# Kernel optimization log

Hardware: AMD Instinct MI355X
Metric: run time of the kernel (lower is better)

## Reference

```python
import jax, jax.numpy as jnp
import numpy as np

B, C, H, W = 8, 64, 64, 64
CI = 32  # inter_channels = in_channels // 2
EPS = 1e-5


def conv1x1(x, w, b=None):
    # x: (b,c,h,w), w: (o,c) -> (b,o,h,w)
    y = jnp.einsum('bchw,oc->bohw', x, w)
    if b is not None:
        y = y + b[None, :, None, None]
    return y


def maxpool2x2(x):
    b, c, h, w = x.shape
    return x.reshape(b, c, h // 2, 2, w // 2, 2).max(axis=(3, 5))


def setup_inputs() -> dict:
    key = jax.random.key(0)
    ks = jax.random.split(key, 12)
    s = 0.05
    return {
        'x': jax.random.normal(ks[0], (B, C, H, W), jnp.float32),
        'theta_w': jax.random.normal(ks[1], (CI, C), jnp.float32) * s,
        'theta_b': jax.random.normal(ks[2], (CI,), jnp.float32) * s,
        'phi_w': jax.random.normal(ks[3], (CI, C), jnp.float32) * s,
        'phi_b': jax.random.normal(ks[4], (CI,), jnp.float32) * s,
        'psi_w': jax.random.normal(ks[5], (CI, C), jnp.float32) * s,
        'psi_b': jax.random.normal(ks[6], (CI,), jnp.float32) * s,
        'cp_w': jax.random.normal(ks[7], (2 * CI,), jnp.float32) * s,  # concat_project 1x1, no bias
        'W_w': jax.random.normal(ks[8], (C, CI + 1), jnp.float32) * s,
        'W_b': jax.random.normal(ks[9], (C,), jnp.float32) * s,
        'bn_gamma': jax.random.normal(ks[10], (C,), jnp.float32) * s + 1.0,
        'bn_beta': jax.random.normal(ks[11], (C,), jnp.float32) * s,
    }


def reference(x, theta_w, theta_b, phi_w, phi_b, psi_w, psi_b, cp_w, W_w, W_b, bn_gamma, bn_beta):
    b = x.shape[0]
    # psi / phi branches get 2x2 maxpool (sub_sample=True default)
    psi_x = maxpool2x2(conv1x1(x, psi_w, psi_b)).reshape(b, CI, -1)      # (b,ci,M)
    psi_x = psi_x.transpose(0, 2, 1)                                     # (b,M,ci)
    theta_x = conv1x1(x, theta_w, theta_b).reshape(b, CI, -1)            # (b,ci,N)
    phi_x = maxpool2x2(conv1x1(x, phi_w, phi_b)).reshape(b, CI, -1)      # (b,ci,M)
    # concat_project(cat[theta_i, phi_j]) + ReLU == relu(w1.theta_i + w2.phi_j)
    w1, w2 = cp_w[:CI], cp_w[CI:]
    a = jnp.einsum('bcn,c->bn', theta_x, w1)                             # (b,N)
    bb = jnp.einsum('bcm,c->bm', phi_x, w2)                              # (b,M)
    f = jax.nn.relu(a[:, :, None] + bb[:, None, :])                      # (b,N,M)
    M = f.shape[-1]
    f_div_C = f / float(M)
    y = jnp.matmul(f_div_C, psi_x)                                       # (b,N,ci)
    y = y.transpose(0, 2, 1).reshape(b, CI, H, W)
    # r_structure_type='zero' -> zero structure channel
    structure_feat = jnp.zeros((b, 1, H, W), y.dtype)
    y = jnp.concatenate([y, structure_feat], axis=1)                     # (b,ci+1,H,W)
    wy = conv1x1(y, W_w, W_b)                                            # (b,C,H,W)
    # BatchNorm2d, training-mode batch stats, biased variance
    mu = wy.mean(axis=(0, 2, 3), keepdims=True)
    var = wy.var(axis=(0, 2, 3), keepdims=True)
    wy = (wy - mu) * jax.lax.rsqrt(var + EPS)
    wy = wy * bn_gamma[None, :, None, None] + bn_beta[None, :, None, None]
    return wy + x
```

## Files before the change

### kernel.cpp

```cpp
#include <hip/hip_runtime.h>

#define OFF_A    0
#define OFF_BB   32768
#define OFF_RK   40960
#define OFF_U    57344
#define OFF_T1   581632
#define OFF_T2   1106432
#define OFF_KK   1631232
#define OFF_MP1  1664000
#define OFF_MP2  1664512
#define OFF_HC   1665024
#define OFF_HS   1673224
#define OFF_HS2  1681424
#define OFF_BAR  1689624

__device__ __forceinline__ void stg(float* p, float v) {
    __hip_atomic_store(p, v, __ATOMIC_RELAXED, __HIP_MEMORY_SCOPE_AGENT);
}
__device__ __forceinline__ float ldg1(const float* p) {
    return __hip_atomic_load(p, __ATOMIC_RELAXED, __HIP_MEMORY_SCOPE_AGENT);
}
__device__ __forceinline__ void stgi(int* p, int v) {
    __hip_atomic_store(p, v, __ATOMIC_RELAXED, __HIP_MEMORY_SCOPE_AGENT);
}
__device__ __forceinline__ int ldgi(const int* p) {
    return __hip_atomic_load(p, __ATOMIC_RELAXED, __HIP_MEMORY_SCOPE_AGENT);
}
__device__ __forceinline__ void stgu(unsigned* p, unsigned v) {
    __hip_atomic_store(p, v, __ATOMIC_RELAXED, __HIP_MEMORY_SCOPE_AGENT);
}
__device__ __forceinline__ unsigned ldgu(const unsigned* p) {
    return __hip_atomic_load(p, __ATOMIC_RELAXED, __HIP_MEMORY_SCOPE_AGENT);
}

__global__ __launch_bounds__(1024) void kA(
    const float* __restrict__ x, const float* __restrict__ theta_w,
    const float* __restrict__ theta_b, const float* __restrict__ phi_w,
    const float* __restrict__ phi_b, const float* __restrict__ psi_w,
    const float* __restrict__ psi_b, const float* __restrict__ cp_w,
    const float* __restrict__ Ww, float* __restrict__ ws)
{
    __shared__ float sh[7524];
    const int tid = threadIdx.x;
    const int bid = blockIdx.x;
    const int b   = bid >> 5;
    const int sub = bid & 31;
    unsigned* bars = (unsigned*)(ws + OFF_BAR);
    float* sA2 = sh + 7396;

    {
        if (bid == 0 && tid == 0) {
            for (int i = 0; i < 8; ++i) stgu(&bars[(i + 1) << 5], 0u);
        }
        if (tid < 97) {
            int e = sub*97 + tid;
            if (e < 1025)      stg(&ws[OFF_HC  + b*1025 + e], 0.0f);
            else if (e < 2050) stg(&ws[OFF_HS  + b*1025 + e - 1025], 0.0f);
            else if (e < 3075) stg(&ws[OFF_HS2 + b*1025 + e - 2050], 0.0f);
        }
        float* sm   = sh;
        float* sth  = sh + 4160;
        float* spsi = sh + 4228;
        float* sWw  = sh + 5284;
        for (int e = tid; e < 2048; e += 1024) {
            int i = e >> 6, c = e & 63;
            sm[i*130 + 2*c]     = phi_w[e];
            sm[i*130 + 2*c + 1] = psi_w[e];
        }
        for (int e = tid; e < 2048; e += 1024)
            sWw[(e >> 5)*33 + (e & 31)] = Ww[(e >> 5)*33 + (e & 31)];
        if (tid < 64) {
            float s = 0;
            for (int i = 0; i < 32; ++i) s += cp_w[i]*theta_w[i*64 + tid];
            sth[tid] = s;
        } else if (tid == 64) {
            float s = 0;
            for (int i = 0; i < 32; ++i) s += cp_w[i]*theta_b[i];
            sth[64] = s;
        }
        __syncthreads();
        if (bid == 0 && tid == 0) {
            stgu(&bars[288], 0x5A5A5A5Au);
            stgu(&bars[289], 0xA5A5A5A5u);
        }
        int i = tid & 31;
        int mIdx = tid >> 5;
        int m = (sub << 5) + mIdx;
        int ph = m >> 5, pw = m & 31;
        const float* xb = x + b*262144 + ph*128 + pw*2;
        const float2* wrow = (const float2*)(sm + i*130);
        float tb = sth[64];
        float p0=0,p1=0,p2=0,p3=0,s0=0,s1=0,s2=0,s3=0;
        float a0=tb,a1=tb,a2=tb,a3=tb;
        #pragma unroll 8
        for (int c = 0; c < 64; ++c) {
            float2 xa = *(const float2*)(xb + c*4096);
            float2 xc = *(const float2*)(xb + c*4096 + 64);
            float2 w  = wrow[c];
            float st  = sth[c];
            p0 += xa.x*w.x; p1 += xa.y*w.x; p2 += xc.x*w.x; p3 += xc.y*w.x;
            s0 += xa.x*w.y; s1 += xa.y*w.y; s2 += xc.x*w.y; s3 += xc.y*w.y;
            a0 += xa.x*st;  a1 += xa.y*st;  a2 += xc.x*st;  a3 += xc.y*st;
        }
        float pv = fmaxf(fmaxf(p0,p1), fmaxf(p2,p3)) + phi_b[i];
        float sv = fmaxf(fmaxf(s0,s1), fmaxf(s2,s3)) + psi_b[i];
        spsi[mIdx*33 + i] = sv;
        float v = pv * cp_w[32 + i];
        v += __shfl_xor(v, 16, 32);
        v += __shfl_xor(v,  8, 32);
        v += __shfl_xor(v,  4, 32);
        v += __shfl_xor(v,  2, 32);
        v += __shfl_xor(v,  1, 32);
        if (i == 0) {
            stg(&ws[OFF_BB + (b<<10) + m], v);
            int nb = (b<<12) + ph*128 + pw*2;
            ws[OFF_A + nb]      = a0;
            ws[OFF_A + nb + 1]  = a1;
            ws[OFF_A + nb + 64] = a2;
            ws[OFF_A + nb + 65] = a3;
            int nl = pw*2;
            sA2[nl]      = a0;
            sA2[nl + 1]  = a1;
            sA2[nl + 64] = a2;
            sA2[nl + 65] = a3;
        }
        __syncthreads();
        #pragma unroll
        for (int rep = 0; rep < 2; ++rep) {
            int o  = (tid >> 5) + (rep << 5);
            int ml = tid & 31;
            const float* pr = &spsi[ml*33];
            const float* wr = &sWw[o*33];
            float u = 0;
            #pragma unroll
            for (int i2 = 0; i2 < 32; ++i2) u += pr[i2]*wr[i2];
            stg(&ws[OFF_U + (((b<<6) + o)<<10) + (sub<<5) + ml], u);
        }
    }
    __syncthreads();
    if (tid == 0) {
        while ((ldgu(&bars[288]) ^ ldgu(&bars[289])) != 0xFFFFFFFFu)
            __builtin_amdgcn_s_sleep(2);
        unsigned* ctr = bars + ((b + 1) << 5);
        __hip_atomic_fetch_add(ctr, 1u, __ATOMIC_RELAXED,
                               __HIP_MEMORY_SCOPE_AGENT);
        while (ldgu(ctr) < 32u) __builtin_amdgcn_s_sleep(2);
    }
    __syncthreads();

    {
        float* sb = sh;
        sb[tid] = ldg1(&ws[OFF_BB + (b<<10) + tid]);
        __syncthreads();
        {
            int ml = tid >> 5, jl = tid & 31;
            int m = (sub << 5) + ml;
            float vv = sb[m];
            int cnt = 0;
            for (int s = 0; s < 32; ++s) {
                int j = jl + (s << 5);
                float u = sb[j];
                cnt += (u > vv || (u == vv && j < m)) ? 1 : 0;
            }
            cnt += __shfl_xor(cnt,  1, 32);
            cnt += __shfl_xor(cnt,  2, 32);
            cnt += __shfl_xor(cnt,  4, 32);
            cnt += __shfl_xor(cnt,  8, 32);
            cnt += __shfl_xor(cnt, 16, 32);
            if (jl == 0)
                stgi(&((int*)ws)[OFF_RK + (b<<10) + m], cnt);
        }
        {
            int l = tid >> 3, jl = tid & 7;
            int n = (sub << 7) + l;
            float av = sA2[l];
            float tt = -av;
            const float2* sb2 = (const float2*)sb;
            int cnt = 0;
            for (int s = 0; s < 64; ++s) {
                float2 u = sb2[jl + (s << 3)];
                cnt += (u.x > tt) ? 1 : 0;
                cnt += (u.y > tt) ? 1 : 0;
            }
            cnt += __shfl_xor(cnt, 1, 8);
            cnt += __shfl_xor(cnt, 2, 8);
            cnt += __shfl_xor(cnt, 4, 8);
            if (jl == 0) {
                ((int*)ws)[OFF_KK + (b<<12) + n] = cnt;
                atomicAdd(&ws[OFF_HC + b*1025 + cnt], 1.0f);
                atomicAdd(&ws[OFF_HS + b*1025 + cnt], av);
                atomicAdd(&ws[OFF_HS2 + b*1025 + cnt], av*av);
            }
        }
    }
    __syncthreads();
    if (tid == 0) {
        unsigned* ctr = bars + ((b + 1) << 5);
        __hip_atomic_fetch_add(ctr, 1u, __ATOMIC_RELAXED,
                               __HIP_MEMORY_SCOPE_AGENT);
        while (ldgu(ctr) < 64u) __builtin_amdgcn_s_sleep(2);
    }
    __syncthreads();

    {
        const int obase = sub << 1;
        float* ssb  = sh;
        float* sU0  = sh + 1024;
        float* sU1  = sh + 2048;
        float* shc  = sh + 3072;
        float* shs  = sh + 4097;
        float* shs2 = sh + 5122;
        float* swp1 = sh + 6148;
        float* swp2 = sh + 6180;
        {
            float bbv = ldg1(&ws[OFF_BB + (b<<10) + tid]);
            int   rk  = ldgi(&((const int*)ws)[OFF_RK + (b<<10) + tid]);
            float u0  = ldg1(&ws[OFF_U + (((b<<6) + obase)<<10) + tid]);
            float u1  = ldg1(&ws[OFF_U + (((b<<6) + obase + 1)<<10) + tid]);
            ssb[rk] = bbv;
            sU0[rk] = u0;
            sU1[rk] = u1;
            shc[tid]  = ldg1(&ws[OFF_HC  + b*1025 + tid]);
            shs[tid]  = ldg1(&ws[OFF_HS  + b*1025 + tid]);
            shs2[tid] = ldg1(&ws[OFF_HS2 + b*1025 + tid]);
            if (tid == 0) {
                shc[1024]  = ldg1(&ws[OFF_HC  + b*1025 + 1024]);
                shs[1024]  = ldg1(&ws[OFF_HS  + b*1025 + 1024]);
                shs2[1024] = ldg1(&ws[OFF_HS2 + b*1025 + 1024]);
            }
        }
        __syncthreads();
        int ch = tid >> 1, o2 = tid & 1;
        int o  = obase + o2;
        int wv = tid >> 6, chl = (tid & 63) >> 1;
        const float* sU = o2 ? sU1 : sU0;
        float p[2], sp[2];
        float s1 = 0, s2 = 0;
        #pragma unroll
        for (int jl = 0; jl < 2; ++jl) {
            int jj = (ch<<1) + jl;
            float v = sU[jj];
            p[jl] = v;
            sp[jl] = ssb[jj]*v;
            s1 += v; s2 += sp[jl];
        }
        float own1 = s1, own2 = s2;
        #pragma unroll
        for (int d = 1; d < 32; d <<= 1) {
            float u1 = __shfl_up(s1, d<<1, 64);
            float u2 = __shfl_up(s2, d<<1, 64);
            if (chl >= d) { s1 += u1; s2 += u2; }
        }
        if (chl == 31) { swp1[(wv<<1)+o2] = s1; swp2[(wv<<1)+o2] = s2; }
        __syncthreads();
        float off1 = 0, off2 = 0;
        for (int w = 0; w < 16; ++w) {
            if (w < wv) { off1 += swp1[(w<<1)+o2]; off2 += swp2[(w<<1)+o2]; }
        }
        float run1 = off1 + s1 - own1;
        float run2 = off2 + s2 - own2;
        float* T1 = ws + OFF_T1 + b*65600;
        float* T2 = ws + OFF_T2 + b*65600;
        if (ch == 0) { T1[o] = 0.0f; T2[o] = 0.0f; }
        const float inv = 1.0f/1024.0f;
        float m1 = 0, m2 = 0;
        #pragma unroll
        for (int jl = 0; jl < 2; ++jl) {
            int k = (ch<<1) + jl + 1;
            run1 += p[jl]; run2 += sp[jl];
            float t1 = run1*inv, t2 = run2*inv;
            T1[(k<<6) + o] = t1;
            T2[(k<<6) + o] = t2;
            float c = shc[k], sa_ = shs[k], sa2 = shs2[k];
            m1 += sa_*t1 + c*t2;
            m2 += (sa2*t1 + 2.0f*sa_*t2)*t1 + c*t2*t2;
        }
        m1 += __shfl_xor(m1,  2, 64); m2 += __shfl_xor(m2,  2, 64);
        m1 += __shfl_xor(m1,  4, 64); m2 += __shfl_xor(m2,  4, 64);
        m1 += __shfl_xor(m1,  8, 64); m2 += __shfl_xor(m2,  8, 64);
        m1 += __shfl_xor(m1, 16, 64); m2 += __shfl_xor(m2, 16, 64);
        m1 += __shfl_xor(m1, 32, 64); m2 += __shfl_xor(m2, 32, 64);
        __syncthreads();
        if (chl == 0) { swp1[(wv<<1)+o2] = m1; swp2[(wv<<1)+o2] = m2; }
        __syncthreads();
        if (tid < 2) {
            float a1 = 0, a2 = 0;
            for (int w = 0; w < 16; ++w) {
                a1 += swp1[(w<<1)+tid]; a2 += swp2[(w<<1)+tid];
            }
            ws[OFF_MP1 + (b<<6) + obase + tid] = a1;
            ws[OFF_MP2 + (b<<6) + obase + tid] = a2;
        }
    }
}

__global__ __launch_bounds__(512) void kB(
    const float* __restrict__ x, const float* __restrict__ Wb,
    const float* __restrict__ gamma, const float* __restrict__ beta,
    const float* __restrict__ ws, float* __restrict__ out)
{
    __shared__ float tile[64*65];
    __shared__ float sa[64];
    __shared__ int   sk[64];
    __shared__ float sA[64];
    __shared__ float sD[64];
    const int tid = threadIdx.x;
    const int b   = blockIdx.x >> 6;
    const int n0  = (blockIdx.x & 63) << 6;
    if (tid < 64) {
        sa[tid] = ws[OFF_A + (b<<12) + n0 + tid];
        sk[tid] = ((const int*)ws)[OFF_KK + (b<<12) + n0 + tid];
        const float Ninv = 1.0f/32768.0f;
        float m1s = 0, m2s = 0;
        #pragma unroll
        for (int b3 = 0; b3 < 8; ++b3) {
            m1s += ws[OFF_MP1 + (b3<<6) + tid];
            m2s += ws[OFF_MP2 + (b3<<6) + tid];
        }
        float m1 = m1s * Ninv;
        float m2 = m2s * Ninv;
        float wb = Wb[tid];
        float mu  = m1 + wb;
        float E2  = m2 + 2.0f*wb*m1 + wb*wb;
        float var = E2 - mu*mu;
        float A = gamma[tid] * rsqrtf(var + 1e-5f);
        sA[tid] = A;
        sD[tid] = beta[tid] + A*(wb - mu);
    }
    __syncthreads();
    const float* T1 = ws + OFF_T1 + b*65600;
    const float* T2 = ws + OFF_T2 + b*65600;
    {
        int o = tid & 63, ng = tid >> 6;
        float Ao = sA[o], Do = sD[o];
        #pragma unroll
        for (int j = 0; j < 8; ++j) {
            int n = (ng << 3) + j;
            int k = sk[n];
            float a = sa[n];
            float t1 = T1[(k<<6) + o];
            float t2 = T2[(k<<6) + o];
            tile[o*65 + n] = Ao*(a*t1 + t2) + Do;
        }
    }
    __syncthreads();
    {
        int n = tid & 63, og = tid >> 6;
        #pragma unroll
        for (int j = 0; j < 8; ++j) {
            int o = (og << 3) + j;
            int idx = ((b<<6) + o)*4096 + n0 + n;
            out[idx] = tile[o*65 + n] + x[idx];
        }
    }
}

extern "C" void kernel_launch(void* const* d_in, const int* in_sizes, int n_in,
                              void* d_out, int out_size, void* d_ws, size_t ws_size,
                              hipStream_t stream)
{
    const float* x       = (const float*)d_in[0];
    const float* theta_w = (const float*)d_in[1];
    const float* theta_b = (const float*)d_in[2];
    const float* phi_w   = (const float*)d_in[3];
    const float* phi_b   = (const float*)d_in[4];
    const float* psi_w   = (const float*)d_in[5];
    const float* psi_b   = (const float*)d_in[6];
    const float* cp_w    = (const float*)d_in[7];
    const float* Ww      = (const float*)d_in[8];
    const float* Wb      = (const float*)d_in[9];
    const float* gamma   = (const float*)d_in[10];
    const float* beta    = (const float*)d_in[11];
    float* ws  = (float*)d_ws;
    float* out = (float*)d_out;

    kA<<<256, 1024, 0, stream>>>(x, theta_w, theta_b, phi_w, phi_b,
                                 psi_w, psi_b, cp_w, Ww, ws);
    kB<<<512, 512, 0, stream>>>(x, Wb, gamma, beta, ws, out);
}
```

Before: 125.6 us.

## Split kA across 512 smaller blocks and interleave T1/T2 as float2

kA now runs 512 blocks of 512 threads. Each block handles 16 pooled positions, and in the prefix-scan phase each block handles one output channel instead of two. Block ids are interleaved across the batch, with matching changes to the per-batch barrier counts and the local A indexing. The T1/T2 tables are merged into one float2 array, so kB's data-dependent gather needs a single 8-byte load per element instead of two scattered loads. The aim is more parallelism and better gather efficiency. The cost is that the spin barriers now wait on twice as many blocks and rely on all 512 blocks being co-resident.

Result: no change. 128.0 us (+1.9%).

```diff
diff --git a/kernel.cpp b/kernel.cpp
--- a/kernel.cpp
+++ b/kernel.cpp
@@ -4,8 +4,7 @@
 #define OFF_BB   32768
 #define OFF_RK   40960
 #define OFF_U    57344
-#define OFF_T1   581632
-#define OFF_T2   1106432
+#define OFF_T12  581632
 #define OFF_KK   1631232
 #define OFF_MP1  1664000
 #define OFF_MP2  1664512
@@ -33,27 +32,27 @@
     return __hip_atomic_load(p, __ATOMIC_RELAXED, __HIP_MEMORY_SCOPE_AGENT);
 }
 
-__global__ __launch_bounds__(1024) void kA(
+__global__ __launch_bounds__(512) void kA(
     const float* __restrict__ x, const float* __restrict__ theta_w,
     const float* __restrict__ theta_b, const float* __restrict__ phi_w,
     const float* __restrict__ phi_b, const float* __restrict__ psi_w,
     const float* __restrict__ psi_b, const float* __restrict__ cp_w,
     const float* __restrict__ Ww, float* __restrict__ ws)
 {
-    __shared__ float sh[7524];
+    __shared__ float sh[6932];
     const int tid = threadIdx.x;
     const int bid = blockIdx.x;
-    const int b   = bid >> 5;
-    const int sub = bid & 31;
+    const int b   = bid & 7;
+    const int sub = bid >> 3;
     unsigned* bars = (unsigned*)(ws + OFF_BAR);
-    float* sA2 = sh + 7396;
+    float* sA2 = sh + 6868;
 
     {
         if (bid == 0 && tid == 0) {
             for (int i = 0; i < 8; ++i) stgu(&bars[(i + 1) << 5], 0u);
         }
-        if (tid < 97) {
-            int e = sub*97 + tid;
+        if (tid < 49) {
+            int e = sub*49 + tid;
             if (e < 1025)      stg(&ws[OFF_HC  + b*1025 + e], 0.0f);
             else if (e < 2050) stg(&ws[OFF_HS  + b*1025 + e - 1025], 0.0f);
             else if (e < 3075) stg(&ws[OFF_HS2 + b*1025 + e - 2050], 0.0f);
@@ -61,13 +60,13 @@
         float* sm   = sh;
         float* sth  = sh + 4160;
         float* spsi = sh + 4228;
-        float* sWw  = sh + 5284;
-        for (int e = tid; e < 2048; e += 1024) {
+        float* sWw  = sh + 4756;
+        for (int e = tid; e < 2048; e += 512) {
             int i = e >> 6, c = e & 63;
             sm[i*130 + 2*c]     = phi_w[e];
             sm[i*130 + 2*c + 1] = psi_w[e];
         }
-        for (int e = tid; e < 2048; e += 1024)
+        for (int e = tid; e < 2048; e += 512)
             sWw[(e >> 5)*33 + (e & 31)] = Ww[(e >> 5)*33 + (e & 31)];
         if (tid < 64) {
             float s = 0;
@@ -85,7 +84,7 @@
         }
         int i = tid & 31;
         int mIdx = tid >> 5;
-        int m = (sub << 5) + mIdx;
+        int m = (sub << 4) + mIdx;
         int ph = m >> 5, pw = m & 31;
         const float* xb = x + b*262144 + ph*128 + pw*2;
         const float2* wrow = (const float2*)(sm + i*130);
@@ -118,23 +117,24 @@
             ws[OFF_A + nb + 1]  = a1;
             ws[OFF_A + nb + 64] = a2;
             ws[OFF_A + nb + 65] = a3;
-            int nl = pw*2;
-            sA2[nl]      = a0;
-            sA2[nl + 1]  = a1;
-            sA2[nl + 64] = a2;
-            sA2[nl + 65] = a3;
+            int pwl = pw & 15;
+            sA2[pwl*2]      = a0;
+            sA2[pwl*2 + 1]  = a1;
+            sA2[32 + pwl*2]     = a2;
+            sA2[32 + pwl*2 + 1] = a3;
         }
         __syncthreads();
         #pragma unroll
         for (int rep = 0; rep < 2; ++rep) {
-            int o  = (tid >> 5) + (rep << 5);
-            int ml = tid & 31;
+            int idx = tid + (rep << 9);
+            int o  = idx >> 4;
+            int ml = idx & 15;
             const float* pr = &spsi[ml*33];
             const float* wr = &sWw[o*33];
             float u = 0;
             #pragma unroll
             for (int i2 = 0; i2 < 32; ++i2) u += pr[i2]*wr[i2];
-            stg(&ws[OFF_U + (((b<<6) + o)<<10) + (sub<<5) + ml], u);
+            stg(&ws[OFF_U + (((b<<6) + o)<<10) + (sub<<4) + ml], u);
         }
     }
     __syncthreads();
@@ -144,17 +144,18 @@
         unsigned* ctr = bars + ((b + 1) << 5);
         __hip_atomic_fetch_add(ctr, 1u, __ATOMIC_RELAXED,
                                __HIP_MEMORY_SCOPE_AGENT);
-        while (ldgu(ctr) < 32u) __builtin_amdgcn_s_sleep(2);
+        while (ldgu(ctr) < 64u) __builtin_amdgcn_s_sleep(2);
     }
     __syncthreads();
 
     {
         float* sb = sh;
-        sb[tid] = ldg1(&ws[OFF_BB + (b<<10) + tid]);
+        for (int e = tid; e < 1024; e += 512)
+            sb[e] = ldg1(&ws[OFF_BB + (b<<10) + e]);
         __syncthreads();
         {
             int ml = tid >> 5, jl = tid & 31;
-            int m = (sub << 5) + ml;
+            int m = (sub << 4) + ml;
             float vv = sb[m];
             int cnt = 0;
             for (int s = 0; s < 32; ++s) {
@@ -172,8 +173,10 @@
         }
         {
             int l = tid >> 3, jl = tid & 7;
-            int n = (sub << 7) + l;
-            float av = sA2[l];
+            int row = l >> 5, col = l & 31;
+            int phb = sub >> 1, half = sub & 1;
+            int n = (2*phb + row)*64 + half*32 + col;
+            float av = sA2[row*32 + col];
             float tt = -av;
             const float2* sb2 = (const float2*)sb;
             int cnt = 0;
@@ -198,42 +201,34 @@
         unsigned* ctr = bars + ((b + 1) << 5);
         __hip_atomic_fetch_add(ctr, 1u, __ATOMIC_RELAXED,
                                __HIP_MEMORY_SCOPE_AGENT);
-        while (ldgu(ctr) < 64u) __builtin_amdgcn_s_sleep(2);
-    }
-    __syncthreads();
-
-    {
-        const int obase = sub << 1;
+        while (ldgu(ctr) < 128u) __builtin_amdgcn_s_sleep(2);
+    }
+    __syncthreads();
+
+    {
+        const int o = sub;
         float* ssb  = sh;
-        float* sU0  = sh + 1024;
-        float* sU1  = sh + 2048;
-        float* shc  = sh + 3072;
-        float* shs  = sh + 4097;
-        float* shs2 = sh + 5122;
-        float* swp1 = sh + 6148;
-        float* swp2 = sh + 6180;
-        {
-            float bbv = ldg1(&ws[OFF_BB + (b<<10) + tid]);
-            int   rk  = ldgi(&((const int*)ws)[OFF_RK + (b<<10) + tid]);
-            float u0  = ldg1(&ws[OFF_U + (((b<<6) + obase)<<10) + tid]);
-            float u1  = ldg1(&ws[OFF_U + (((b<<6) + obase + 1)<<10) + tid]);
+        float* sU   = sh + 1024;
+        float* shc  = sh + 2048;
+        float* shs  = sh + 3073;
+        float* shs2 = sh + 4098;
+        float* swp1 = sh + 5123;
+        float* swp2 = sh + 5131;
+        for (int e = tid; e < 1024; e += 512) {
+            float bbv = ldg1(&ws[OFF_BB + (b<<10) + e]);
+            int   rk  = ldgi(&((const int*)ws)[OFF_RK + (b<<10) + e]);
+            float u   = ldg1(&ws[OFF_U + (((b<<6) + o)<<10) + e]);
             ssb[rk] = bbv;
-            sU0[rk] = u0;
-            sU1[rk] = u1;
-            shc[tid]  = ldg1(&ws[OFF_HC  + b*1025 + tid]);
-            shs[tid]  = ldg1(&ws[OFF_HS  + b*1025 + tid]);
-            shs2[tid] = ldg1(&ws[OFF_HS2 + b*1025 + tid]);
-            if (tid == 0) {
-                shc[1024]  = ldg1(&ws[OFF_HC  + b*1025 + 1024]);
-                shs[1024]  = ldg1(&ws[OFF_HS  + b*1025 + 1024]);
-                shs2[1024] = ldg1(&ws[OFF_HS2 + b*1025 + 1024]);
-            }
-        }
-        __syncthreads();
-        int ch = tid >> 1, o2 = tid & 1;
-        int o  = obase + o2;
-        int wv = tid >> 6, chl = (tid & 63) >> 1;
-        const float* sU = o2 ? sU1 : sU0;
+            sU[rk]  = u;
+        }
+        for (int e = tid; e < 1025; e += 512) {
+            shc[e]  = ldg1(&ws[OFF_HC  + b*1025 + e]);
+            shs[e]  = ldg1(&ws[OFF_HS  + b*1025 + e]);
+            shs2[e] = ldg1(&ws[OFF_HS2 + b*1025 + e]);
+        }
+        __syncthreads();
+        int ch = tid;
+        int chl = tid & 63, wv = tid >> 6;
         float p[2], sp[2];
         float s1 = 0, s2 = 0;
         #pragma unroll
@@ -246,22 +241,21 @@
         }
         float own1 = s1, own2 = s2;
         #pragma unroll
-        for (int d = 1; d < 32; d <<= 1) {
-            float u1 = __shfl_up(s1, d<<1, 64);
-            float u2 = __shfl_up(s2, d<<1, 64);
+        for (int d = 1; d < 64; d <<= 1) {
+            float u1 = __shfl_up(s1, d, 64);
+            float u2 = __shfl_up(s2, d, 64);
             if (chl >= d) { s1 += u1; s2 += u2; }
         }
-        if (chl == 31) { swp1[(wv<<1)+o2] = s1; swp2[(wv<<1)+o2] = s2; }
+        if (chl == 63) { swp1[wv] = s1; swp2[wv] = s2; }
         __syncthreads();
         float off1 = 0, off2 = 0;
-        for (int w = 0; w < 16; ++w) {
-            if (w < wv) { off1 += swp1[(w<<1)+o2]; off2 += swp2[(w<<1)+o2]; }
+        for (int w = 0; w < 8; ++w) {
+            if (w < wv) { off1 += swp1[w]; off2 += swp2[w]; }
         }
         float run1 = off1 + s1 - own1;
         float run2 = off2 + s2 - own2;
-        float* T1 = ws + OFF_T1 + b*65600;
-        float* T2 = ws + OFF_T2 + b*65600;
-        if (ch == 0) { T1[o] = 0.0f; T2[o] = 0.0f; }
+        float2* T12 = (float2*)(ws + OFF_T12) + (size_t)b*65600;
+        if (ch == 0) T12[o] = make_float2(0.0f, 0.0f);
         const float inv = 1.0f/1024.0f;
         float m1 = 0, m2 = 0;
         #pragma unroll
@@ -269,27 +263,25 @@
             int k = (ch<<1) + jl + 1;
             run1 += p[jl]; run2 += sp[jl];
             float t1 = run1*inv, t2 = run2*inv;
-            T1[(k<<6) + o] = t1;
-            T2[(k<<6) + o] = t2;
+            T12[(k<<6) + o] = make_float2(t1, t2);
             float c = shc[k], sa_ = shs[k], sa2 = shs2[k];
             m1 += sa_*t1 + c*t2;
             m2 += (sa2*t1 + 2.0f*sa_*t2)*t1 + c*t2*t2;
         }
+        m1 += __shfl_xor(m1,  1, 64); m2 += __shfl_xor(m2,  1, 64);
         m1 += __shfl_xor(m1,  2, 64); m2 += __shfl_xor(m2,  2, 64);
         m1 += __shfl_xor(m1,  4, 64); m2 += __shfl_xor(m2,  4, 64);
         m1 += __shfl_xor(m1,  8, 64); m2 += __shfl_xor(m2,  8, 64);
         m1 += __shfl_xor(m1, 16, 64); m2 += __shfl_xor(m2, 16, 64);
         m1 += __shfl_xor(m1, 32, 64); m2 += __shfl_xor(m2, 32, 64);
         __syncthreads();
-        if (chl == 0) { swp1[(wv<<1)+o2] = m1; swp2[(wv<<1)+o2] = m2; }
-        __syncthreads();
-        if (tid < 2) {
+        if (chl == 0) { swp1[wv] = m1; swp2[wv] = m2; }
+        __syncthreads();
+        if (tid == 0) {
             float a1 = 0, a2 = 0;
-            for (int w = 0; w < 16; ++w) {
-                a1 += swp1[(w<<1)+tid]; a2 += swp2[(w<<1)+tid];
-            }
-            ws[OFF_MP1 + (b<<6) + obase + tid] = a1;
-            ws[OFF_MP2 + (b<<6) + obase + tid] = a2;
+            for (int w = 0; w < 8; ++w) { a1 += swp1[w]; a2 += swp2[w]; }
+            ws[OFF_MP1 + (b<<6) + o] = a1;
+            ws[OFF_MP2 + (b<<6) + o] = a2;
         }
     }
 }
@@ -305,8 +297,8 @@
     __shared__ float sA[64];
     __shared__ float sD[64];
     const int tid = threadIdx.x;
-    const int b   = blockIdx.x >> 6;
-    const int n0  = (blockIdx.x & 63) << 6;
+    const int b   = blockIdx.x & 7;
+    const int n0  = (blockIdx.x >> 3) << 6;
     if (tid < 64) {
         sa[tid] = ws[OFF_A + (b<<12) + n0 + tid];
         sk[tid] = ((const int*)ws)[OFF_KK + (b<<12) + n0 + tid];
@@ -328,8 +320,7 @@
         sD[tid] = beta[tid] + A*(wb - mu);
     }
     __syncthreads();
-    const float* T1 = ws + OFF_T1 + b*65600;
-    const float* T2 = ws + OFF_T2 + b*65600;
+    const float2* T12 = (const float2*)(ws + OFF_T12) + (size_t)b*65600;
     {
         int o = tid & 63, ng = tid >> 6;
         float Ao = sA[o], Do = sD[o];
@@ -338,9 +329,8 @@
             int n = (ng << 3) + j;
             int k = sk[n];
             float a = sa[n];
-            float t1 = T1[(k<<6) + o];
-            float t2 = T2[(k<<6) + o];
-            tile[o*65 + n] = Ao*(a*t1 + t2) + Do;
+            float2 t = T12[(k<<6) + o];
+            tile[o*65 + n] = Ao*(a*t.x + t.y) + Do;
         }
     }
     __syncthreads();
@@ -374,7 +364,7 @@
     float* ws  = (float*)d_ws;
     float* out = (float*)d_out;
 
-    kA<<<256, 1024, 0, stream>>>(x, theta_w, theta_b, phi_w, phi_b,
-                                 psi_w, psi_b, cp_w, Ww, ws);
+    kA<<<512, 512, 0, stream>>>(x, theta_w, theta_b, phi_w, phi_b,
+                                psi_w, psi_b, cp_w, Ww, ws);
     kB<<<512, 512, 0, stream>>>(x, Wb, gamma, beta, ws, out);
 }
```

## Stage x tile in shared memory and reorganize phi/psi conv work per thread

Applied to the files above, without the earlier changes.

The first phase of kA now loads the block's 2-row x tile (64 channels × 128 pixels) into LDS with float4 loads. Each thread then computes 4 output features for 2 pixels from LDS instead of reading x redundantly from global memory for every feature. Max-pooling uses a lane shuffle plus a vertical max, and the phi projection reduction moves to a separate pass after a barrier. This cuts the 32-fold redundant global reads of x. In exchange it uses more LDS, adds a barrier, and computes theta on only one warp group, which leaves the other lanes idle.

Result: faster. 115.7 us (-7.9%).

```diff
diff --git a/kernel.cpp b/kernel.cpp
--- a/kernel.cpp
+++ b/kernel.cpp
@@ -40,13 +40,16 @@
     const float* __restrict__ psi_b, const float* __restrict__ cp_w,
     const float* __restrict__ Ww, float* __restrict__ ws)
 {
-    __shared__ float sh[7524];
+    __shared__ __align__(16) float sh[12484];
     const int tid = threadIdx.x;
     const int bid = blockIdx.x;
     const int b   = bid >> 5;
     const int sub = bid & 31;
     unsigned* bars = (unsigned*)(ws + OFF_BAR);
-    float* sA2 = sh + 7396;
+    float* sX  = sh;
+    float* sW  = sh + 8192;
+    float* sth = sh + 12288;
+    float* sA2 = sh + 12356;
 
     {
         if (bid == 0 && tid == 0) {
@@ -58,17 +61,20 @@
             else if (e < 2050) stg(&ws[OFF_HS  + b*1025 + e - 1025], 0.0f);
             else if (e < 3075) stg(&ws[OFF_HS2 + b*1025 + e - 2050], 0.0f);
         }
-        float* sm   = sh;
-        float* sth  = sh + 4160;
-        float* spsi = sh + 4228;
-        float* sWw  = sh + 5284;
-        for (int e = tid; e < 2048; e += 1024) {
-            int i = e >> 6, c = e & 63;
-            sm[i*130 + 2*c]     = phi_w[e];
-            sm[i*130 + 2*c + 1] = psi_w[e];
-        }
-        for (int e = tid; e < 2048; e += 1024)
-            sWw[(e >> 5)*33 + (e & 31)] = Ww[(e >> 5)*33 + (e & 31)];
+        {
+            const float4* x4 = (const float4*)x;
+            float4* sX4 = (float4*)sX;
+            #pragma unroll
+            for (int e = tid; e < 2048; e += 1024) {
+                int c = e >> 5, off = e & 31;
+                sX4[e] = x4[b*65536 + c*1024 + sub*32 + off];
+            }
+        }
+        #pragma unroll
+        for (int e = tid; e < 4096; e += 1024) {
+            int f = e >> 6, c = e & 63;
+            sW[c*64 + f] = (f < 32) ? phi_w[f*64 + c] : psi_w[(f-32)*64 + c];
+        }
         if (tid < 64) {
             float s = 0;
             for (int i = 0; i < 32; ++i) s += cp_w[i]*theta_w[i*64 + tid];
@@ -83,48 +89,75 @@
             stgu(&bars[288], 0x5A5A5A5Au);
             stgu(&bars[289], 0xA5A5A5A5u);
         }
-        int i = tid & 31;
-        int mIdx = tid >> 5;
-        int m = (sub << 5) + mIdx;
-        int ph = m >> 5, pw = m & 31;
-        const float* xb = x + b*262144 + ph*128 + pw*2;
-        const float2* wrow = (const float2*)(sm + i*130);
+        const int pxl = tid & 63;
+        const int fg  = tid >> 6;
         float tb = sth[64];
-        float p0=0,p1=0,p2=0,p3=0,s0=0,s1=0,s2=0,s3=0;
-        float a0=tb,a1=tb,a2=tb,a3=tb;
+        float a00=0, a01=0, a02=0, a03=0;
+        float a10=0, a11=0, a12=0, a13=0;
+        float th0 = tb, th1 = tb;
+        const float4* sW4 = (const float4*)sW;
         #pragma unroll 8
         for (int c = 0; c < 64; ++c) {
-            float2 xa = *(const float2*)(xb + c*4096);
-            float2 xc = *(const float2*)(xb + c*4096 + 64);
-            float2 w  = wrow[c];
-            float st  = sth[c];
-            p0 += xa.x*w.x; p1 += xa.y*w.x; p2 += xc.x*w.x; p3 += xc.y*w.x;
-            s0 += xa.x*w.y; s1 += xa.y*w.y; s2 += xc.x*w.y; s3 += xc.y*w.y;
-            a0 += xa.x*st;  a1 += xa.y*st;  a2 += xc.x*st;  a3 += xc.y*st;
-        }
-        float pv = fmaxf(fmaxf(p0,p1), fmaxf(p2,p3)) + phi_b[i];
-        float sv = fmaxf(fmaxf(s0,s1), fmaxf(s2,s3)) + psi_b[i];
-        spsi[mIdx*33 + i] = sv;
-        float v = pv * cp_w[32 + i];
-        v += __shfl_xor(v, 16, 32);
-        v += __shfl_xor(v,  8, 32);
-        v += __shfl_xor(v,  4, 32);
-        v += __shfl_xor(v,  2, 32);
-        v += __shfl_xor(v,  1, 32);
-        if (i == 0) {
-            stg(&ws[OFF_BB + (b<<10) + m], v);
-            int nb = (b<<12) + ph*128 + pw*2;
-            ws[OFF_A + nb]      = a0;
-            ws[OFF_A + nb + 1]  = a1;
-            ws[OFF_A + nb + 64] = a2;
-            ws[OFF_A + nb + 65] = a3;
-            int nl = pw*2;
-            sA2[nl]      = a0;
-            sA2[nl + 1]  = a1;
-            sA2[nl + 64] = a2;
-            sA2[nl + 65] = a3;
-        }
-        __syncthreads();
+            float x0 = sX[c*128 + pxl];
+            float x1 = sX[c*128 + 64 + pxl];
+            float4 w = sW4[c*16 + fg];
+            a00 += x0*w.x; a01 += x0*w.y; a02 += x0*w.z; a03 += x0*w.w;
+            a10 += x1*w.x; a11 += x1*w.y; a12 += x1*w.z; a13 += x1*w.w;
+            if (fg == 0) {
+                float st = sth[c];
+                th0 += x0*st; th1 += x1*st;
+            }
+        }
+        __syncthreads();
+        float* spsi = sh;
+        float* sphi = sh + 1056;
+        float* sWw  = sh + 2112;
+        {
+            float v0 = fmaxf(a00, a10), v1 = fmaxf(a01, a11);
+            float v2 = fmaxf(a02, a12), v3 = fmaxf(a03, a13);
+            float h0 = fmaxf(v0, __shfl_xor(v0, 1, 64));
+            float h1 = fmaxf(v1, __shfl_xor(v1, 1, 64));
+            float h2 = fmaxf(v2, __shfl_xor(v2, 1, 64));
+            float h3 = fmaxf(v3, __shfl_xor(v3, 1, 64));
+            if ((pxl & 1) == 0) {
+                int ml = pxl >> 1;
+                int f0 = fg << 2;
+                if (fg < 8) {
+                    sphi[ml*33 + f0]     = h0 + phi_b[f0];
+                    sphi[ml*33 + f0 + 1] = h1 + phi_b[f0 + 1];
+                    sphi[ml*33 + f0 + 2] = h2 + phi_b[f0 + 2];
+                    sphi[ml*33 + f0 + 3] = h3 + phi_b[f0 + 3];
+                } else {
+                    int i0 = f0 - 32;
+                    spsi[ml*33 + i0]     = h0 + psi_b[i0];
+                    spsi[ml*33 + i0 + 1] = h1 + psi_b[i0 + 1];
+                    spsi[ml*33 + i0 + 2] = h2 + psi_b[i0 + 2];
+                    spsi[ml*33 + i0 + 3] = h3 + psi_b[i0 + 3];
+                }
+            }
+        }
+        if (fg == 0) {
+            int nb = (b<<12) + (sub<<7);
+            ws[OFF_A + nb + pxl]      = th0;
+            ws[OFF_A + nb + 64 + pxl] = th1;
+            sA2[pxl]      = th0;
+            sA2[64 + pxl] = th1;
+        }
+        #pragma unroll
+        for (int e = tid; e < 2048; e += 1024)
+            sWw[(e >> 5)*33 + (e & 31)] = Ww[(e >> 5)*33 + (e & 31)];
+        __syncthreads();
+        {
+            int ml = tid >> 5, il = tid & 31;
+            float v = sphi[ml*33 + il] * cp_w[32 + il];
+            v += __shfl_xor(v, 16, 32);
+            v += __shfl_xor(v,  8, 32);
+            v += __shfl_xor(v,  4, 32);
+            v += __shfl_xor(v,  2, 32);
+            v += __shfl_xor(v,  1, 32);
+            if (il == 0)
+                stg(&ws[OFF_BB + (b<<10) + (sub<<5) + ml], v);
+        }
         #pragma unroll
         for (int rep = 0; rep < 2; ++rep) {
             int o  = (tid >> 5) + (rep << 5);
```
